# Kernel optimization log

Hardware: AMD Instinct MI355X
Metric: run time of the kernel (lower is better)

Reference implementation:

```python
import jax, jax.numpy as jnp
import numpy as np

B, SEQ, C_IN, D_MODEL = 64, 1534, 21, 516
M, TAU, KS, PAD, NK = 7, 3, 8, 21, 74  # kernel_size=m+1, pad=m*tau, num_kernels=74


def _sinusoid(n, d):
    # matches PositionalEmbedding / FixedEmbedding table construction
    pos = np.arange(n, dtype=np.float32)[:, None]
    div = np.exp(np.arange(0, d, 2, dtype=np.float32) * (-np.log(10000.0) / d))
    tab = np.zeros((n, d), dtype=np.float32)
    tab[:, 0::2] = np.sin(pos * div)
    tab[:, 1::2] = np.cos(pos * div)
    return jnp.asarray(tab)


def setup_inputs() -> dict:
    key = jax.random.key(0)
    k1, k2, k3 = jax.random.split(key, 3)
    x = jax.random.normal(k1, (B, SEQ, C_IN), dtype=jnp.float32)
    x_mark = jax.random.randint(k2, (B, SEQ, 5), 0, 4)
    kernels = jax.random.normal(k3, (NK, KS), dtype=jnp.float32)
    return {
        'x': x,
        'x_mark': x_mark,
        'kernels': kernels,
        'pe': _sinusoid(SEQ, D_MODEL),
        'hour_tab': _sinusoid(24, D_MODEL),
        'weekday_tab': _sinusoid(7, D_MODEL),
        'day_tab': _sinusoid(32, D_MODEL),
        'month_tab': _sinusoid(13, D_MODEL),
    }


def _token_embed(x, kernels):
    # Fuses the Python loop of 74 grouped conv1d launches into two einsums.
    b, L, c = x.shape
    xp = jnp.pad(x.transpose(0, 2, 1), ((0, 0), (0, 0), (PAD, 0)))  # [B,C,L+PAD]
    nw = (L + PAD - KS) // TAU + 1                                   # number of windows W
    idx = jnp.arange(nw)[:, None] * TAU + jnp.arange(KS)[None, :]    # [W,KS]
    win = xp[:, :, idx]                                              # [B,C,W,KS]
    # 73 depthwise kernels applied to every channel; concat order is kernel-major
    main = jnp.einsum('bcwk,nk->bwnc', win, kernels[:NK - 1]).reshape(b, nw, (NK - 1) * c)
    # last kernel applied to one randomly chosen channel (fixed to 0 for determinism)
    fin = jnp.einsum('bwk,k->bw', win[:, 0], kernels[NK - 1])[..., None]
    comb = jnp.concatenate([main, fin], axis=-1)                     # [B,W,73*C+1]
    return comb.transpose(0, 2, 1)[:, :, :L]                         # [B,73*C+1,W]


def reference(x, x_mark, kernels, pe, hour_tab, weekday_tab, day_tab, month_tab):
    L = x.shape[1]
    tok = _token_embed(x, kernels)                                   # [B, SEQ, D_MODEL]
    xm = x_mark.astype(jnp.int32)
    temp = (hour_tab[xm[:, :, 3]] + weekday_tab[xm[:, :, 2]]
            + day_tab[xm[:, :, 1]] + month_tab[xm[:, :, 0]])          # [B, SEQ, D_MODEL]
    # dropout in eval mode = identity
    return tok + pe[None, :L, :] + temp
```

## Files before the change

### kernel.cpp

```cpp
#include <hip/hip_runtime.h>

#define BATCH   64
#define SEQ     1534
#define C_IN    21
#define DM      516
#define NJ      129
#define KS      8
#define NK      74
#define PADL    21
#define NSPLIT  4
#define JW      12
#define NBJ     11
#define TSPAN   (12*(JW-1) + 17)

__global__ __launch_bounds__(256) void embed_kernel(
    const float* __restrict__ x,
    const int*   __restrict__ xm,
    const float* __restrict__ kernels,
    const float* __restrict__ pe,
    const float* __restrict__ hour_tab,
    const float* __restrict__ weekday_tab,
    const float* __restrict__ day_tab,
    const float* __restrict__ month_tab,
    float*       __restrict__ out)
{
    __shared__ float sk[NK * KS];
    __shared__ float sx[TSPAN * C_IN];

    const int bid = blockIdx.x;
    const int s   = bid % NSPLIT;
    const int t1  = bid / NSPLIT;
    const int jb  = t1 % NBJ;
    const int b   = t1 / NBJ;
    const int j0  = jb * JW;
    const int t0  = 12 * j0 - PADL;

    for (int t = threadIdx.x; t < NK * KS; t += 256) sk[t] = kernels[t];

    {
        const int base = (b * SEQ + t0) * C_IN;
        const int lo   = -t0 * C_IN;
        const int hi   = (SEQ - t0) * C_IN;
        for (int p = threadIdx.x; p < TSPAN * C_IN; p += 256) {
            float v = 0.0f;
            if (p >= lo && p < hi) v = x[base + p];
            sx[p] = v;
        }
    }
    __syncthreads();

    const int ch = threadIdx.x / JW;
    const int jj = threadIdx.x % JW;
    const int j  = j0 + jj;
    if (ch >= C_IN || j >= NJ) return;

    float w[17];
#pragma unroll
    for (int u = 0; u < 17; ++u) w[u] = sx[(12 * jj + u) * C_IN + ch];

    const float4* pe4 = (const float4*)pe;
    const float4* h4  = (const float4*)hour_tab;
    const float4* wd4 = (const float4*)weekday_tab;
    const float4* dy4 = (const float4*)day_tab;
    const float4* mo4 = (const float4*)month_tab;
    float4*       o4  = (float4*)out;

    const int bSEQ = b * SEQ;

    for (int n = s; n < NK; n += NSPLIT) {
        if (n == NK - 1 && ch != 0) continue;
        const int i = n * C_IN + ch;

        float acc[4];
#pragma unroll
        for (int dd = 0; dd < 4; ++dd) {
            float a = 0.0f;
#pragma unroll
            for (int k = 0; k < KS; ++k) a += w[3 * dd + k] * sk[n * KS + k];
            acc[dd] = a;
        }

        const int* xr = xm + (bSEQ + i) * 5;
        const int hi = xr[3], wi = xr[2], di = xr[1], mi = xr[0];

        const float4 p  = pe4[i * NJ + j];
        const float4 th = h4 [hi * NJ + j];
        const float4 tw = wd4[wi * NJ + j];
        const float4 td = dy4[di * NJ + j];
        const float4 tm = mo4[mi * NJ + j];

        float4 o;
        o.x = acc[0] + p.x + th.x + tw.x + td.x + tm.x;
        o.y = acc[1] + p.y + th.y + tw.y + td.y + tm.y;
        o.z = acc[2] + p.z + th.z + tw.z + td.z + tm.z;
        o.w = acc[3] + p.w + th.w + tw.w + td.w + tm.w;

        o4[(bSEQ + i) * NJ + j] = o;
    }
}

extern "C" void kernel_launch(void* const* d_in, const int* in_sizes, int n_in,
                              void* d_out, int out_size, void* d_ws, size_t ws_size,
                              hipStream_t stream) {
    const float* x        = (const float*)d_in[0];
    const int*   x_mark   = (const int*)  d_in[1];
    const float* kernels  = (const float*)d_in[2];
    const float* pe       = (const float*)d_in[3];
    const float* hour_tab = (const float*)d_in[4];
    const float* wday_tab = (const float*)d_in[5];
    const float* day_tab  = (const float*)d_in[6];
    const float* mon_tab  = (const float*)d_in[7];
    float*       out      = (float*)d_out;

    const int blocks = BATCH * NBJ * NSPLIT;
    embed_kernel<<<blocks, 256, 0, stream>>>(
        x, x_mark, kernels, pe, hour_tab, wday_tab, day_tab, mon_tab, out);
}
```

Baseline: 283.0 us.

## Stage temporal tables and x_mark indices in LDS, use nontemporal output stores

```diff
diff --git a/kernel.cpp b/kernel.cpp
--- a/kernel.cpp
+++ b/kernel.cpp
@@ -12,6 +12,10 @@
 #define JW      12
 #define NBJ     11
 #define TSPAN   (12*(JW-1) + 17)
+#define TROWS   ((NK + NSPLIT - 1) / NSPLIT)
+#define TABROWS 76
+
+typedef float f32x4 __attribute__((ext_vector_type(4)));
 
 __global__ __launch_bounds__(256) void embed_kernel(
     const float* __restrict__ x,
@@ -24,8 +28,10 @@
     const float* __restrict__ month_tab,
     float*       __restrict__ out)
 {
-    __shared__ float sk[NK * KS];
-    __shared__ float sx[TSPAN * C_IN];
+    __shared__ float  sk[NK * KS];
+    __shared__ float  sx[TSPAN * C_IN];
+    __shared__ float4 stab[TABROWS * JW];
+    __shared__ int4   sxm[TROWS * C_IN];
 
     const int bid = blockIdx.x;
     const int s   = bid % NSPLIT;
@@ -34,17 +40,51 @@
     const int b   = t1 / NBJ;
     const int j0  = jb * JW;
     const int t0  = 12 * j0 - PADL;
+    const int bSEQ = b * SEQ;
+    const int nmax = (NK - 1 - s) / NSPLIT + 1;
 
     for (int t = threadIdx.x; t < NK * KS; t += 256) sk[t] = kernels[t];
 
     {
-        const int base = (b * SEQ + t0) * C_IN;
+        const int base = (bSEQ + t0) * C_IN;
         const int lo   = -t0 * C_IN;
         const int hi   = (SEQ - t0) * C_IN;
         for (int p = threadIdx.x; p < TSPAN * C_IN; p += 256) {
             float v = 0.0f;
             if (p >= lo && p < hi) v = x[base + p];
             sx[p] = v;
+        }
+    }
+
+    {
+        const int jlim = NJ - j0;
+        for (int q = threadIdx.x; q < TABROWS * JW; q += 256) {
+            const int r  = q / JW;
+            const int jj = q % JW;
+            float4 v = make_float4(0.f, 0.f, 0.f, 0.f);
+            if (jj < jlim) {
+                const float4* src; int rr;
+                if (r < 24)      { src = (const float4*)hour_tab;    rr = r; }
+                else if (r < 31) { src = (const float4*)weekday_tab; rr = r - 24; }
+                else if (r < 63) { src = (const float4*)day_tab;     rr = r - 31; }
+                else             { src = (const float4*)month_tab;   rr = r - 63; }
+                v = src[rr * NJ + j0 + jj];
+            }
+            stab[q] = v;
+        }
+    }
+
+    {
+        int* sxmi = (int*)sxm;
+        for (int p = threadIdx.x; p < nmax * C_IN * 4; p += 256) {
+            const int q   = p & 3;
+            const int idx = p >> 2;
+            const int chh = idx % C_IN;
+            const int n   = s + NSPLIT * (idx / C_IN);
+            const int i   = n * C_IN + chh;
+            int v = 0;
+            if (i < SEQ) v = xm[(bSEQ + i) * 5 + q];
+            sxmi[p] = v;
         }
     }
     __syncthreads();
@@ -59,15 +99,10 @@
     for (int u = 0; u < 17; ++u) w[u] = sx[(12 * jj + u) * C_IN + ch];
 
     const float4* pe4 = (const float4*)pe;
-    const float4* h4  = (const float4*)hour_tab;
-    const float4* wd4 = (const float4*)weekday_tab;
-    const float4* dy4 = (const float4*)day_tab;
-    const float4* mo4 = (const float4*)month_tab;
     float4*       o4  = (float4*)out;
 
-    const int bSEQ = b * SEQ;
-
-    for (int n = s; n < NK; n += NSPLIT) {
+    for (int t = 0; t < nmax; ++t) {
+        const int n = s + NSPLIT * t;
         if (n == NK - 1 && ch != 0) continue;
         const int i = n * C_IN + ch;
 
@@ -80,22 +115,21 @@
             acc[dd] = a;
         }
 
-        const int* xr = xm + (bSEQ + i) * 5;
-        const int hi = xr[3], wi = xr[2], di = xr[1], mi = xr[0];
+        const int4 xi = sxm[t * C_IN + ch];
 
         const float4 p  = pe4[i * NJ + j];
-        const float4 th = h4 [hi * NJ + j];
-        const float4 tw = wd4[wi * NJ + j];
-        const float4 td = dy4[di * NJ + j];
-        const float4 tm = mo4[mi * NJ + j];
+        const float4 th = stab[ xi.w        * JW + jj];
+        const float4 tw = stab[(24 + xi.z)  * JW + jj];
+        const float4 td = stab[(31 + xi.y)  * JW + jj];
+        const float4 tm = stab[(63 + xi.x)  * JW + jj];
 
-        float4 o;
+        f32x4 o;
         o.x = acc[0] + p.x + th.x + tw.x + td.x + tm.x;
         o.y = acc[1] + p.y + th.y + tw.y + td.y + tm.y;
         o.z = acc[2] + p.z + th.z + tw.z + td.z + tm.z;
         o.w = acc[3] + p.w + th.w + tw.w + td.w + tm.w;
 
-        o4[(bSEQ + i) * NJ + j] = o;
+        __builtin_nontemporal_store(o, (f32x4*)&o4[(bSEQ + i) * NJ + j]);
     }
 }
 
```

Result: slower. 321.2 us (+13.5%).
